# Kernel tuning notes

Hardware: AMD Instinct MI355X
Metric: run time of the kernel (lower is better)

The kernel has to match this reference:

```python
import jax, jax.numpy as jnp
import numpy as np
from jax import lax

B, T, N, H, D = 256, 512, 256, 256, 2  # batch, steps, substrate dim, controller hidden, delay depth
WASHOUT = 64


def setup_inputs() -> dict:
    key = jax.random.key(0)
    ks = jax.random.split(key, 12)
    def w(k, shape, fan_in):
        return (jax.random.normal(k, shape, dtype=jnp.float32) / np.float32(np.sqrt(fan_in)))
    return {
        "settings_seq": jax.random.randint(ks[0], (B, T, 2), 0, 2, dtype=jnp.int32),
        "noise_seq_A": 0.1 * jax.random.normal(ks[1], (B, T, N), dtype=jnp.float32),
        "noise_seq_B": 0.1 * jax.random.normal(ks[2], (B, T, N), dtype=jnp.float32),
        # substrate (two echo-state reservoirs), per-side input = [setting_bit, delayed_logit]
        "W_in_A": w(ks[3], (2, N), 2),
        "W_rec_A": w(ks[4], (N, N), N),
        "W_in_B": w(ks[5], (2, N), 2),
        "W_rec_B": w(ks[6], (N, N), N),
        # controller: single GRU cell over concat(state_A, state_B, spin_A, spin_B) + linear head -> 2 logits
        "Wx": w(ks[7], (2 * N + 2, 3 * H), 2 * N + 2),
        "Wh": w(ks[8], (H, 3 * H), H),
        "b_gru": jnp.zeros((3 * H,), jnp.float32),
        "Wout": w(ks[9], (H, 2), H),
        "b_out": jnp.zeros((2,), jnp.float32),
        "T_total": T,
        "washout_steps": WASHOUT,
    }


def reference(settings_seq, noise_seq_A, noise_seq_B,
              W_in_A, W_rec_A, W_in_B, W_rec_B,
              Wx, Wh, b_gru, Wout, b_out,
              T_total, washout_steps):
    bsz = settings_seq.shape[0]
    h0 = jnp.zeros((bsz, H), jnp.float32)  # controller thought state starts at zeros each step (R <= 1 branch)

    def gru_cell(x, h):
        gx = x @ Wx + b_gru            # [B, 3H]
        gh = h @ Wh                    # [B, 3H] (zero contribution when h == 0)
        z = jax.nn.sigmoid(gx[:, :H] + gh[:, :H])
        r = jax.nn.sigmoid(gx[:, H:2 * H] + gh[:, H:2 * H])
        n = jnp.tanh(gx[:, 2 * H:] + r * gh[:, 2 * H:])
        return (1.0 - z) * n + z * h

    def step(carry, xs):
        sA, sB, buf = carry            # states [B,N], delay buffer [D,B,2]
        nA_t, nB_t, set_t = xs
        bits = set_t.astype(jnp.float32)          # [B,2]
        spins = 2.0 * bits - 1.0                  # bits_to_spins
        x = jnp.concatenate([sA + nA_t, sB + nB_t, spins], axis=-1)
        h = gru_cell(x, h0)
        logits = h @ Wout + b_out                 # [B,2]
        delayed = buf[0]                          # logits from D steps ago
        buf = jnp.concatenate([buf[1:], logits[None]], axis=0)
        inA = jnp.stack([bits[:, 0], delayed[:, 0]], axis=-1)  # [B,2]
        inB = jnp.stack([bits[:, 1], delayed[:, 1]], axis=-1)
        sA = jnp.tanh(inA @ W_in_A + sA @ W_rec_A)
        sB = jnp.tanh(inB @ W_in_B + sB @ W_rec_B)
        return (sA, sB, buf), (jnp.sign(logits), bits)

    init = (jnp.zeros((bsz, N), jnp.float32),
            jnp.zeros((bsz, N), jnp.float32),
            jnp.zeros((D, bsz, 2), jnp.float32))
    xs = (jnp.transpose(noise_seq_A, (1, 0, 2)),
          jnp.transpose(noise_seq_B, (1, 0, 2)),
          jnp.transpose(settings_seq, (1, 0, 2)))
    _, (signs, bits_log) = lax.scan(step, init, xs, length=T_total)
    signs = jnp.transpose(signs, (1, 0, 2))[:, washout_steps:]          # [B, T-washout, 2]
    settings_log = jnp.transpose(bits_log, (1, 0, 2))[:, washout_steps:]
    return signs[..., 0], signs[..., 1], settings_log
```

## Files before the change

kernel.cpp:

```cpp
#include <hip/hip_runtime.h>
#include <cmath>

#define B_ 256
#define T_ 512
#define WASH 64
#define TOUT 448
#define NT 512
#define NBLK 256

#define SRING_OFF 0
#define LRING_OFF 524288
#define SFLAG_OFF 532480
#define LFLAG_OFF 536576

__global__ void init_kernel(float* ws) {
    const int i = blockIdx.x * blockDim.x + threadIdx.x;
    if (i < 8192)
        __hip_atomic_store((unsigned*)(ws + SFLAG_OFF) + i, 0u,
                           __ATOMIC_RELAXED, __HIP_MEMORY_SCOPE_AGENT);
}

__global__ void __launch_bounds__(NT, 2)
loop_kernel(const int* __restrict__ settings, const float* __restrict__ noiseA,
            const float* __restrict__ noiseB, const float* __restrict__ WinA,
            const float* __restrict__ WrecA, const float* __restrict__ WinB,
            const float* __restrict__ WrecB, const float* __restrict__ Wx,
            const float* __restrict__ bg, const float* __restrict__ Wout,
            const float* __restrict__ bout, float* __restrict__ out, float* ws)
{
    __shared__ float part[8][64][17];
    __shared__ float xbuf[516][8];
    __shared__ float sloc[256][4];
    __shared__ float hz[64][9];
    __shared__ float hn[64][9];
    __shared__ float bitsf[4];
    __shared__ float dlybuf[4];

    const int tid = threadIdx.x;
    const int bid = blockIdx.x;
    unsigned* sflag = (unsigned*)(ws + SFLAG_OFF);
    unsigned* lflag = (unsigned*)(ws + LFLAG_OFF);
    float* sring = ws + SRING_OFF;
    float* lring = ws + LRING_OFF;
    float* out0 = out;
    float* out1 = out + (size_t)B_ * TOUT;
    float* out2 = out + (size_t)2 * B_ * TOUT;

    if (bid < 128) {
        const int side = bid & 1, rg4 = bid >> 1;
        const int r0 = rg4 * 4, rg8 = rg4 >> 1, row8b = (rg4 & 1) * 4;
        const int kq = tid >> 6, cg = tid & 63;
        const float* Wr = side ? WrecB : WrecA;
        const float* Wi = side ? WinB : WinA;

        float4 w[32];
        #pragma unroll
        for (int i = 0; i < 32; ++i)
            w[i] = *(const float4*)(Wr + (size_t)(kq * 32 + i) * 256 + cg * 4);

        const int col = tid >> 1, rp = (tid & 1) * 2;
        const float win0 = Wi[col], win1 = Wi[256 + col];
        const float bo = bout[side];

        for (int i = tid; i < 1024; i += NT) ((float*)sloc)[i] = 0.f;
        __syncthreads();

        for (int t = 0; t < T_ + 2; ++t) {
            if (t >= 2 && tid < 4) {
                unsigned* f = lflag + (rg8 * 4 + tid) * 32;
                int g = 0;
                while (__hip_atomic_load(f, __ATOMIC_RELAXED, __HIP_MEMORY_SCOPE_AGENT)
                       < (unsigned)(t - 1)) {
                    __builtin_amdgcn_s_sleep(1);
                    if (++g > 80000) break;
                }
            }
            __syncthreads();

            if (tid < 4) {
                bitsf[tid] = (t < T_)
                    ? (float)settings[((size_t)(r0 + tid) * T_ + t) * 2 + side] : 0.f;
            } else if (tid < 8) {
                const int rr = tid - 4;
                float s = 0.f;
                if (t >= 2) {
                    const float* lb = lring + ((((size_t)((t - 2) & 3)) * 32 + rg8) * 4) * 16
                                      + (row8b + rr) * 2 + side;
                    #pragma unroll
                    for (int cb = 0; cb < 4; ++cb)
                        s += __hip_atomic_load(lb + cb * 16, __ATOMIC_RELAXED,
                                               __HIP_MEMORY_SCOPE_AGENT);
                    s += bo;
                    if (t - 2 >= WASH) {
                        const float sg = (s > 0.f) ? 1.f : ((s < 0.f) ? -1.f : 0.f);
                        __builtin_nontemporal_store(sg,
                            (side ? out1 : out0) + (size_t)(r0 + rr) * TOUT + (t - 2 - WASH));
                    }
                }
                dlybuf[rr] = s;
            }
            if (t < T_) {
                float a00=0,a01=0,a02=0,a03=0, a10=0,a11=0,a12=0,a13=0;
                float a20=0,a21=0,a22=0,a23=0, a30=0,a31=0,a32=0,a33=0;
                #pragma unroll
                for (int i = 0; i < 32; ++i) {
                    const float4 w4 = w[i];
                    const float4 s4 = *(const float4*)&sloc[kq * 32 + i][0];
                    a00 = fmaf(s4.x, w4.x, a00); a10 = fmaf(s4.y, w4.x, a10);
                    a20 = fmaf(s4.z, w4.x, a20); a30 = fmaf(s4.w, w4.x, a30);
                    a01 = fmaf(s4.x, w4.y, a01); a11 = fmaf(s4.y, w4.y, a11);
                    a21 = fmaf(s4.z, w4.y, a21); a31 = fmaf(s4.w, w4.y, a31);
                    a02 = fmaf(s4.x, w4.z, a02); a12 = fmaf(s4.y, w4.z, a12);
                    a22 = fmaf(s4.z, w4.z, a22); a32 = fmaf(s4.w, w4.z, a32);
                    a03 = fmaf(s4.x, w4.w, a03); a13 = fmaf(s4.y, w4.w, a13);
                    a23 = fmaf(s4.z, w4.w, a23); a33 = fmaf(s4.w, w4.w, a33);
                }
                float* pb = &part[kq][cg][0];
                pb[0]=a00; pb[1]=a10; pb[2]=a20; pb[3]=a30;
                pb[4]=a01; pb[5]=a11; pb[6]=a21; pb[7]=a31;
                pb[8]=a02; pb[9]=a12; pb[10]=a22; pb[11]=a32;
                pb[12]=a03; pb[13]=a13; pb[14]=a23; pb[15]=a33;
            }
            __syncthreads();

            if (t < T_) {
                #pragma unroll
                for (int r = 0; r < 2; ++r) {
                    float e = 0.f;
                    #pragma unroll
                    for (int q = 0; q < 8; ++q)
                        e += part[q][col >> 2][(col & 3) * 4 + rp + r];
                    e += bitsf[rp + r] * win0 + dlybuf[rp + r] * win1;
                    sloc[col][rp + r] = tanhf(e);
                }
            }
            __syncthreads();

            if (t < T_) {
                #pragma unroll
                for (int e = 0; e < 2; ++e) {
                    const int idx = tid + e * NT;
                    const int prow = idx >> 8, pcol = idx & 255;
                    __hip_atomic_store(
                        sring + ((size_t)(((t + 1) & 3) * 2 + side) * 256 + r0 + prow) * 256 + pcol,
                        sloc[pcol][prow], __ATOMIC_RELAXED, __HIP_MEMORY_SCOPE_AGENT);
                }
            }
            __syncthreads();
            if (t < T_ && tid == 0) {
                asm volatile("s_waitcnt vmcnt(0)" ::: "memory");
                __hip_atomic_fetch_add(sflag + (side * 64 + rg4) * 32, 1u,
                                       __ATOMIC_RELAXED, __HIP_MEMORY_SCOPE_AGENT);
            }
        }
    } else {
        const int g = bid - 128, rg8 = g >> 2, cb = g & 3, r0 = rg8 * 8;
        const int kq = tid >> 6, c2 = tid & 63;
        const int zcol = cb * 64 + c2, ncol = 512 + zcol;

        float wz[66], wn[66];
        #pragma unroll
        for (int i = 0; i < 66; ++i) {
            const int k = kq * 64 + i;
            const bool v = (i < 64) || (kq == 7);
            wz[i] = v ? Wx[(size_t)k * 768 + zcol] : 0.f;
            wn[i] = v ? Wx[(size_t)k * 768 + ncol] : 0.f;
        }
        const int hd = tid >> 3, rs4 = (tid >> 1) & 3, zn = tid & 1;
        const float bgr = zn ? bg[512 + cb * 64 + hd] : bg[cb * 64 + hd];
        const int wv = tid >> 6, lane = tid & 63, lj = wv & 1;
        const float wo = Wout[(cb * 64 + lane) * 2 + lj];

        const int xk = tid;
        const int sd = (xk < 256) ? 0 : 1;
        const int nc0 = xk & 255;
        const float* npb = (sd ? noiseB : noiseA)
                           + (size_t)r0 * T_ * 256 + nc0;
        float nz[8];
        #pragma unroll
        for (int r = 0; r < 8; ++r) nz[r] = npb[(size_t)r * T_ * 256];

        for (int u = 0; u < T_; ++u) {
            if (u > 0 && tid < 4) {
                unsigned* f = sflag + ((tid & 1) * 64 + rg8 * 2 + (tid >> 1)) * 32;
                int gg = 0;
                while (__hip_atomic_load(f, __ATOMIC_RELAXED, __HIP_MEMORY_SCOPE_AGENT)
                       < (unsigned)u) {
                    __builtin_amdgcn_s_sleep(1);
                    if (++gg > 80000) break;
                }
            }
            __syncthreads();

            {
                float sv[8];
                #pragma unroll
                for (int r = 0; r < 8; ++r) sv[r] = 0.f;
                if (u > 0) {
                    const float* sb = sring
                        + ((size_t)((u & 3) * 2 + sd) * 256 + r0) * 256 + nc0;
                    #pragma unroll
                    for (int r = 0; r < 8; ++r)
                        sv[r] = __hip_atomic_load(sb + (size_t)r * 256,
                                                  __ATOMIC_RELAXED, __HIP_MEMORY_SCOPE_AGENT);
                }
                const int b = (xk >> 2) & 1;
                *(float4*)&xbuf[xk][4 * b] =
                    make_float4(sv[0] + nz[0], sv[1] + nz[1], sv[2] + nz[2], sv[3] + nz[3]);
                *(float4*)&xbuf[xk][4 - 4 * b] =
                    make_float4(sv[4] + nz[4], sv[5] + nz[5], sv[6] + nz[6], sv[7] + nz[7]);
            }
            if (tid < 16) {
                const int rr = tid >> 1, jj = tid & 1;
                const int bv = settings[((size_t)(r0 + rr) * T_ + u) * 2 + jj];
                xbuf[512 + jj][rr] = 2.f * (float)bv - 1.f;
                if (cb == 0 && u >= WASH)
                    __builtin_nontemporal_store((float)bv,
                        out2 + ((size_t)(r0 + rr) * TOUT + (u - WASH)) * 2 + jj);
            }
            __syncthreads();

            {
                const int un = (u + 1 < T_) ? u + 1 : u;
                #pragma unroll
                for (int r = 0; r < 8; ++r)
                    nz[r] = npb[(size_t)r * T_ * 256 + (size_t)un * 256];

                float az0=0,az1=0,az2=0,az3=0,az4=0,az5=0,az6=0,az7=0;
                float an0=0,an1=0,an2=0,an3=0,an4=0,an5=0,an6=0,an7=0;
                #pragma unroll
                for (int i = 0; i < 66; ++i) {
                    const int k = kq * 64 + i;
                    const int bsw = (k >> 2) & 1;
                    const float4 xa = *(const float4*)&xbuf[k][4 * bsw];
                    const float4 xb = *(const float4*)&xbuf[k][4 - 4 * bsw];
                    const float wzi = wz[i], wni = wn[i];
                    az0 = fmaf(xa.x, wzi, az0); az1 = fmaf(xa.y, wzi, az1);
                    az2 = fmaf(xa.z, wzi, az2); az3 = fmaf(xa.w, wzi, az3);
                    az4 = fmaf(xb.x, wzi, az4); az5 = fmaf(xb.y, wzi, az5);
                    az6 = fmaf(xb.z, wzi, az6); az7 = fmaf(xb.w, wzi, az7);
                    an0 = fmaf(xa.x, wni, an0); an1 = fmaf(xa.y, wni, an1);
                    an2 = fmaf(xa.z, wni, an2); an3 = fmaf(xa.w, wni, an3);
                    an4 = fmaf(xb.x, wni, an4); an5 = fmaf(xb.y, wni, an5);
                    an6 = fmaf(xb.z, wni, an6); an7 = fmaf(xb.w, wni, an7);
                }
                float* pb = &part[kq][c2][0];
                pb[0]=az0;  pb[1]=an0;  pb[2]=az1;  pb[3]=an1;
                pb[4]=az2;  pb[5]=an2;  pb[6]=az3;  pb[7]=an3;
                pb[8]=az4;  pb[9]=an4;  pb[10]=az5; pb[11]=an5;
                pb[12]=az6; pb[13]=an6; pb[14]=az7; pb[15]=an7;
            }
            __syncthreads();

            {
                #pragma unroll
                for (int h = 0; h < 2; ++h) {
                    const int rsub = rs4 + h * 4;
                    float e = bgr;
                    #pragma unroll
                    for (int q = 0; q < 8; ++q) e += part[q][hd][rsub * 2 + zn];
                    if (zn == 0) hz[hd][rsub] = 1.f / (1.f + expf(-e));
                    else         hn[hd][rsub] = tanhf(e);
                }
            }
            __syncthreads();

            {
                #pragma unroll
                for (int h = 0; h < 2; ++h) {
                    const int lrow2 = (wv >> 1) + h * 4;
                    float p = (1.f - hz[lane][lrow2]) * hn[lane][lrow2] * wo;
                    #pragma unroll
                    for (int s = 32; s; s >>= 1) p += __shfl_down(p, s, 64);
                    if (lane == 0)
                        __hip_atomic_store(
                            lring + (((size_t)(u & 3) * 32 + rg8) * 4 + cb) * 16 + lrow2 * 2 + lj,
                            p, __ATOMIC_RELAXED, __HIP_MEMORY_SCOPE_AGENT);
                }
            }
            __syncthreads();
            if (tid == 0) {
                asm volatile("s_waitcnt vmcnt(0)" ::: "memory");
                __hip_atomic_fetch_add(lflag + (rg8 * 4 + cb) * 32, 1u,
                                       __ATOMIC_RELAXED, __HIP_MEMORY_SCOPE_AGENT);
            }
        }
    }
}

extern "C" void kernel_launch(void* const* d_in, const int* in_sizes, int n_in,
                              void* d_out, int out_size, void* d_ws, size_t ws_size,
                              hipStream_t stream) {
    (void)in_sizes; (void)n_in; (void)ws_size; (void)out_size;
    float* ws = (float*)d_ws;
    hipLaunchKernelGGL(init_kernel, dim3(32), dim3(256), 0, stream, ws);

    const int*   settings = (const int*)d_in[0];
    const float* noiseA   = (const float*)d_in[1];
    const float* noiseB   = (const float*)d_in[2];
    const float* WinA     = (const float*)d_in[3];
    const float* WrecA    = (const float*)d_in[4];
    const float* WinB     = (const float*)d_in[5];
    const float* WrecB    = (const float*)d_in[6];
    const float* Wx       = (const float*)d_in[7];
    const float* bg       = (const float*)d_in[9];
    const float* Wout     = (const float*)d_in[10];
    const float* bout     = (const float*)d_in[11];
    float*       outp     = (float*)d_out;

    void* args[] = { &settings, &noiseA, &noiseB, &WinA, &WrecA, &WinB, &WrecB,
                     &Wx, &bg, &Wout, &bout, &outp, &ws };
    hipLaunchCooperativeKernel((void*)loop_kernel, dim3(NBLK), dim3(NT),
                               args, 0, stream);
}
```

Before: 3.790 ms.

## Retile GRU gate matvec to 2 columns per thread with 16-way K split

Changes the GRU controller blocks' matvec mapping so each thread owns two z and two n columns over 32 (instead of 64) K rows, with 16 K-partitions. Each xbuf float4 load now feeds 32 FMAs instead of 16, cutting LDS read traffic per FMA. In exchange the partial-sum buffer is larger, and the reduction stage must sum 16 partials instead of 8. Register count per thread changes (136 weights plus 32 accumulators), which may pressure occupancy under the 2-blocks launch bound.

```diff
diff --git a/kernel.cpp b/kernel.cpp
--- a/kernel.cpp
+++ b/kernel.cpp
@@ -28,7 +28,7 @@
             const float* __restrict__ bg, const float* __restrict__ Wout,
             const float* __restrict__ bout, float* __restrict__ out, float* ws)
 {
-    __shared__ float part[8][64][17];
+    __shared__ float part_raw[16 * 32 * 33];
     __shared__ float xbuf[516][8];
     __shared__ float sloc[256][4];
     __shared__ float hz[64][9];
@@ -47,6 +47,7 @@
     float* out2 = out + (size_t)2 * B_ * TOUT;
 
     if (bid < 128) {
+        float (*part)[64][17] = (float (*)[64][17])part_raw;
         const int side = bid & 1, rg4 = bid >> 1;
         const int r0 = rg4 * 4, rg8 = rg4 >> 1, row8b = (rg4 & 1) * 4;
         const int kq = tid >> 6, cg = tid & 63;
@@ -154,20 +155,26 @@
             }
         }
     } else {
+        float (*partG)[32][33] = (float (*)[32][33])part_raw;
         const int g = bid - 128, rg8 = g >> 2, cb = g & 3, r0 = rg8 * 8;
-        const int kq = tid >> 6, c2 = tid & 63;
-        const int zcol = cb * 64 + c2, ncol = 512 + zcol;
-
-        float wz[66], wn[66];
+        const int kq = tid >> 5, cg = tid & 31;
+        const int zc0 = cb * 64 + 2 * cg;
+        const int nc0_ = 512 + zc0;
+
+        float wz0[34], wz1[34], wn0[34], wn1[34];
         #pragma unroll
-        for (int i = 0; i < 66; ++i) {
-            const int k = kq * 64 + i;
-            const bool v = (i < 64) || (kq == 7);
-            wz[i] = v ? Wx[(size_t)k * 768 + zcol] : 0.f;
-            wn[i] = v ? Wx[(size_t)k * 768 + ncol] : 0.f;
+        for (int i = 0; i < 34; ++i) {
+            const int k = kq * 32 + i;
+            const bool v = (i < 32) || (kq == 15);
+            wz0[i] = v ? Wx[(size_t)k * 768 + zc0]      : 0.f;
+            wz1[i] = v ? Wx[(size_t)k * 768 + zc0 + 1]  : 0.f;
+            wn0[i] = v ? Wx[(size_t)k * 768 + nc0_]     : 0.f;
+            wn1[i] = v ? Wx[(size_t)k * 768 + nc0_ + 1] : 0.f;
         }
         const int hd = tid >> 3, rs4 = (tid >> 1) & 3, zn = tid & 1;
         const float bgr = zn ? bg[512 + cb * 64 + hd] : bg[cb * 64 + hd];
+        const int rcg = hd >> 1;
+        const int rci = (zn ? 2 : 0) + (hd & 1);
         const int wv = tid >> 6, lane = tid & 63, lj = wv & 1;
         const float wo = Wout[(cb * 64 + lane) * 2 + lj];
 
@@ -226,29 +233,33 @@
                 for (int r = 0; r < 8; ++r)
                     nz[r] = npb[(size_t)r * T_ * 256 + (size_t)un * 256];
 
-                float az0=0,az1=0,az2=0,az3=0,az4=0,az5=0,az6=0,az7=0;
-                float an0=0,an1=0,an2=0,an3=0,an4=0,an5=0,an6=0,an7=0;
-                #pragma unroll
-                for (int i = 0; i < 66; ++i) {
-                    const int k = kq * 64 + i;
+                float acc[4][8];
+                #pragma unroll
+                for (int c = 0; c < 4; ++c)
+                    #pragma unroll
+                    for (int r = 0; r < 8; ++r) acc[c][r] = 0.f;
+
+                #pragma unroll
+                for (int i = 0; i < 34; ++i) {
+                    const int k = kq * 32 + i;
                     const int bsw = (k >> 2) & 1;
                     const float4 xa = *(const float4*)&xbuf[k][4 * bsw];
                     const float4 xb = *(const float4*)&xbuf[k][4 - 4 * bsw];
-                    const float wzi = wz[i], wni = wn[i];
-                    az0 = fmaf(xa.x, wzi, az0); az1 = fmaf(xa.y, wzi, az1);
-                    az2 = fmaf(xa.z, wzi, az2); az3 = fmaf(xa.w, wzi, az3);
-                    az4 = fmaf(xb.x, wzi, az4); az5 = fmaf(xb.y, wzi, az5);
-                    az6 = fmaf(xb.z, wzi, az6); az7 = fmaf(xb.w, wzi, az7);
-                    an0 = fmaf(xa.x, wni, an0); an1 = fmaf(xa.y, wni, an1);
-                    an2 = fmaf(xa.z, wni, an2); an3 = fmaf(xa.w, wni, an3);
-                    an4 = fmaf(xb.x, wni, an4); an5 = fmaf(xb.y, wni, an5);
-                    an6 = fmaf(xb.z, wni, an6); an7 = fmaf(xb.w, wni, an7);
-                }
-                float* pb = &part[kq][c2][0];
-                pb[0]=az0;  pb[1]=an0;  pb[2]=az1;  pb[3]=an1;
-                pb[4]=az2;  pb[5]=an2;  pb[6]=az3;  pb[7]=an3;
-                pb[8]=az4;  pb[9]=an4;  pb[10]=az5; pb[11]=an5;
-                pb[12]=az6; pb[13]=an6; pb[14]=az7; pb[15]=an7;
+                    const float xr[8] = { xa.x, xa.y, xa.z, xa.w,
+                                          xb.x, xb.y, xb.z, xb.w };
+                    const float wv4[4] = { wz0[i], wz1[i], wn0[i], wn1[i] };
+                    #pragma unroll
+                    for (int c = 0; c < 4; ++c)
+                        #pragma unroll
+                        for (int r = 0; r < 8; ++r)
+                            acc[c][r] = fmaf(xr[r], wv4[c], acc[c][r]);
+                }
+                float* pb = &partG[kq][cg][0];
+                #pragma unroll
+                for (int c = 0; c < 4; ++c)
+                    #pragma unroll
+                    for (int r = 0; r < 8; ++r)
+                        pb[c * 8 + r] = acc[c][r];
             }
             __syncthreads();
 
@@ -258,7 +269,8 @@
                     const int rsub = rs4 + h * 4;
                     float e = bgr;
                     #pragma unroll
-                    for (int q = 0; q < 8; ++q) e += part[q][hd][rsub * 2 + zn];
+                    for (int q = 0; q < 16; ++q)
+                        e += partG[q][rcg][rci * 8 + rsub];
                     if (zn == 0) hz[hd][rsub] = 1.f / (1.f + expf(-e));
                     else         hn[hd][rsub] = tanhf(e);
                 }
```

Result: slower. 8.987 ms (+137.2%).

## Speculatively prefetch next-step substrate state in GRU blocks and cache flag polls

Applied to the files above, without the earlier changes.

The GRU blocks now poll the substrate ready-flags during the current step's matvec. When all four flags already show the next step is ready, they load the next substrate state and settings and fill xbuf in the tail of the current iteration. This removes the separate spin-wait, the global load phase and one barrier from the next iteration. Both block types also cache the last observed flag value so they skip polling when the producer is known to be ahead. The cost is extra control logic and registers for the prefetched values, with a fallback to the original blocking path when the data is not ready.

```diff
diff --git a/kernel.cpp b/kernel.cpp
--- a/kernel.cpp
+++ b/kernel.cpp
@@ -28,13 +28,14 @@
             const float* __restrict__ bg, const float* __restrict__ Wout,
             const float* __restrict__ bout, float* __restrict__ out, float* ws)
 {
-    __shared__ float part[8][64][17];
+    __shared__ float part_raw[8 * 64 * 17];
     __shared__ float xbuf[516][8];
     __shared__ float sloc[256][4];
     __shared__ float hz[64][9];
     __shared__ float hn[64][9];
     __shared__ float bitsf[4];
     __shared__ float dlybuf[4];
+    __shared__ int   grdy[4];
 
     const int tid = threadIdx.x;
     const int bid = blockIdx.x;
@@ -47,6 +48,7 @@
     float* out2 = out + (size_t)2 * B_ * TOUT;
 
     if (bid < 128) {
+        float (*part)[64][17] = (float (*)[64][17])part_raw;
         const int side = bid & 1, rg4 = bid >> 1;
         const int r0 = rg4 * 4, rg8 = rg4 >> 1, row8b = (rg4 & 1) * 4;
         const int kq = tid >> 6, cg = tid & 63;
@@ -65,11 +67,13 @@
         for (int i = tid; i < 1024; i += NT) ((float*)sloc)[i] = 0.f;
         __syncthreads();
 
+        unsigned lcache = 0;
         for (int t = 0; t < T_ + 2; ++t) {
-            if (t >= 2 && tid < 4) {
+            if (t >= 2 && tid < 4 && lcache < (unsigned)(t - 1)) {
                 unsigned* f = lflag + (rg8 * 4 + tid) * 32;
                 int g = 0;
-                while (__hip_atomic_load(f, __ATOMIC_RELAXED, __HIP_MEMORY_SCOPE_AGENT)
+                while ((lcache = __hip_atomic_load(f, __ATOMIC_RELAXED,
+                                                   __HIP_MEMORY_SCOPE_AGENT))
                        < (unsigned)(t - 1)) {
                     __builtin_amdgcn_s_sleep(1);
                     if (++g > 80000) break;
@@ -154,6 +158,7 @@
             }
         }
     } else {
+        float (*partG)[64][17] = (float (*)[64][17])part_raw;
         const int g = bid - 128, rg8 = g >> 2, cb = g & 3, r0 = rg8 * 8;
         const int kq = tid >> 6, c2 = tid & 63;
         const int zcol = cb * 64 + c2, ncol = 512 + zcol;
@@ -174,57 +179,76 @@
         const int xk = tid;
         const int sd = (xk < 256) ? 0 : 1;
         const int nc0 = xk & 255;
-        const float* npb = (sd ? noiseB : noiseA)
-                           + (size_t)r0 * T_ * 256 + nc0;
+        const float* npb = (sd ? noiseB : noiseA) + (size_t)r0 * T_ * 256 + nc0;
         float nz[8];
         #pragma unroll
         for (int r = 0; r < 8; ++r) nz[r] = npb[(size_t)r * T_ * 256];
 
+        unsigned* myf = sflag + (((tid & 1) * 64) + rg8 * 2 + ((tid >> 1) & 1)) * 32;
+        unsigned scache = 0;
+
+        {
+            const int b = (xk >> 2) & 1;
+            *(float4*)&xbuf[xk][4 * b]     = make_float4(nz[0], nz[1], nz[2], nz[3]);
+            *(float4*)&xbuf[xk][4 - 4 * b] = make_float4(nz[4], nz[5], nz[6], nz[7]);
+        }
+        int sreg = 0;
+        if (tid < 16) {
+            const int rr = tid >> 1, jj = tid & 1;
+            sreg = settings[((size_t)(r0 + rr) * T_) * 2 + jj];
+            xbuf[512 + jj][rr] = 2.f * (float)sreg - 1.f;
+        }
+        __syncthreads();
+        bool rdy = true;
+
         for (int u = 0; u < T_; ++u) {
-            if (u > 0 && tid < 4) {
-                unsigned* f = sflag + ((tid & 1) * 64 + rg8 * 2 + (tid >> 1)) * 32;
-                int gg = 0;
-                while (__hip_atomic_load(f, __ATOMIC_RELAXED, __HIP_MEMORY_SCOPE_AGENT)
-                       < (unsigned)u) {
-                    __builtin_amdgcn_s_sleep(1);
-                    if (++gg > 80000) break;
-                }
-            }
-            __syncthreads();
-
-            {
-                float sv[8];
-                #pragma unroll
-                for (int r = 0; r < 8; ++r) sv[r] = 0.f;
-                if (u > 0) {
+            if (!rdy) {
+                if (tid < 4 && scache < (unsigned)u) {
+                    int gg = 0;
+                    while ((scache = __hip_atomic_load(myf, __ATOMIC_RELAXED,
+                                                       __HIP_MEMORY_SCOPE_AGENT))
+                           < (unsigned)u) {
+                        __builtin_amdgcn_s_sleep(1);
+                        if (++gg > 80000) break;
+                    }
+                }
+                __syncthreads();
+                {
                     const float* sb = sring
                         + ((size_t)((u & 3) * 2 + sd) * 256 + r0) * 256 + nc0;
+                    float sv[8];
                     #pragma unroll
                     for (int r = 0; r < 8; ++r)
                         sv[r] = __hip_atomic_load(sb + (size_t)r * 256,
                                                   __ATOMIC_RELAXED, __HIP_MEMORY_SCOPE_AGENT);
-                }
-                const int b = (xk >> 2) & 1;
-                *(float4*)&xbuf[xk][4 * b] =
-                    make_float4(sv[0] + nz[0], sv[1] + nz[1], sv[2] + nz[2], sv[3] + nz[3]);
-                *(float4*)&xbuf[xk][4 - 4 * b] =
-                    make_float4(sv[4] + nz[4], sv[5] + nz[5], sv[6] + nz[6], sv[7] + nz[7]);
-            }
-            if (tid < 16) {
-                const int rr = tid >> 1, jj = tid & 1;
-                const int bv = settings[((size_t)(r0 + rr) * T_ + u) * 2 + jj];
-                xbuf[512 + jj][rr] = 2.f * (float)bv - 1.f;
-                if (cb == 0 && u >= WASH)
-                    __builtin_nontemporal_store((float)bv,
-                        out2 + ((size_t)(r0 + rr) * TOUT + (u - WASH)) * 2 + jj);
-            }
-            __syncthreads();
+                    const int b = (xk >> 2) & 1;
+                    *(float4*)&xbuf[xk][4 * b] =
+                        make_float4(sv[0] + nz[0], sv[1] + nz[1], sv[2] + nz[2], sv[3] + nz[3]);
+                    *(float4*)&xbuf[xk][4 - 4 * b] =
+                        make_float4(sv[4] + nz[4], sv[5] + nz[5], sv[6] + nz[6], sv[7] + nz[7]);
+                }
+                if (tid < 16) {
+                    const int rr = tid >> 1, jj = tid & 1;
+                    xbuf[512 + jj][rr] = 2.f * (float)sreg - 1.f;
+                    if (cb == 0 && u >= WASH)
+                        __builtin_nontemporal_store((float)sreg,
+                            out2 + ((size_t)(r0 + rr) * TOUT + (u - WASH)) * 2 + jj);
+                }
+                __syncthreads();
+            }
 
             {
                 const int un = (u + 1 < T_) ? u + 1 : u;
                 #pragma unroll
                 for (int r = 0; r < 8; ++r)
                     nz[r] = npb[(size_t)r * T_ * 256 + (size_t)un * 256];
+                if (tid < 16 && u + 1 < T_) {
+                    const int rr = tid >> 1, jj = tid & 1;
+                    sreg = settings[((size_t)(r0 + rr) * T_ + (u + 1)) * 2 + jj];
+                }
+                if (tid < 4 && scache < (unsigned)(u + 1))
+                    scache = __hip_atomic_load(myf, __ATOMIC_RELAXED,
+                                               __HIP_MEMORY_SCOPE_AGENT);
 
                 float az0=0,az1=0,az2=0,az3=0,az4=0,az5=0,az6=0,az7=0;
                 float an0=0,an1=0,an2=0,an3=0,an4=0,an5=0,an6=0,an7=0;
@@ -244,21 +268,33 @@
                     an4 = fmaf(xb.x, wni, an4); an5 = fmaf(xb.y, wni, an5);
                     an6 = fmaf(xb.z, wni, an6); an7 = fmaf(xb.w, wni, an7);
                 }
-                float* pb = &part[kq][c2][0];
+                float* pb = &partG[kq][c2][0];
                 pb[0]=az0;  pb[1]=an0;  pb[2]=az1;  pb[3]=an1;
                 pb[4]=az2;  pb[5]=an2;  pb[6]=az3;  pb[7]=an3;
                 pb[8]=az4;  pb[9]=an4;  pb[10]=az5; pb[11]=an5;
                 pb[12]=az6; pb[13]=an6; pb[14]=az7; pb[15]=an7;
-            }
-            __syncthreads();
-
+                if (tid < 4) grdy[tid] = (scache >= (unsigned)(u + 1)) ? 1 : 0;
+            }
+            __syncthreads();
+
+            const bool rdyn = (u + 1 < T_) &&
+                              grdy[0] && grdy[1] && grdy[2] && grdy[3];
+            float sv[8];
+            if (rdyn) {
+                const float* sb = sring
+                    + ((size_t)(((u + 1) & 3) * 2 + sd) * 256 + r0) * 256 + nc0;
+                #pragma unroll
+                for (int r = 0; r < 8; ++r)
+                    sv[r] = __hip_atomic_load(sb + (size_t)r * 256,
+                                              __ATOMIC_RELAXED, __HIP_MEMORY_SCOPE_AGENT);
+            }
             {
                 #pragma unroll
                 for (int h = 0; h < 2; ++h) {
                     const int rsub = rs4 + h * 4;
                     float e = bgr;
                     #pragma unroll
-                    for (int q = 0; q < 8; ++q) e += part[q][hd][rsub * 2 + zn];
+                    for (int q = 0; q < 8; ++q) e += partG[q][hd][rsub * 2 + zn];
                     if (zn == 0) hz[hd][rsub] = 1.f / (1.f + expf(-e));
                     else         hn[hd][rsub] = tanhf(e);
                 }
@@ -278,12 +314,27 @@
                             p, __ATOMIC_RELAXED, __HIP_MEMORY_SCOPE_AGENT);
                 }
             }
+            if (rdyn) {
+                const int b = (xk >> 2) & 1;
+                *(float4*)&xbuf[xk][4 * b] =
+                    make_float4(sv[0] + nz[0], sv[1] + nz[1], sv[2] + nz[2], sv[3] + nz[3]);
+                *(float4*)&xbuf[xk][4 - 4 * b] =
+                    make_float4(sv[4] + nz[4], sv[5] + nz[5], sv[6] + nz[6], sv[7] + nz[7]);
+                if (tid < 16) {
+                    const int rr = tid >> 1, jj = tid & 1;
+                    xbuf[512 + jj][rr] = 2.f * (float)sreg - 1.f;
+                    if (cb == 0 && u + 1 >= WASH)
+                        __builtin_nontemporal_store((float)sreg,
+                            out2 + ((size_t)(r0 + rr) * TOUT + (u + 1 - WASH)) * 2 + jj);
+                }
+            }
             __syncthreads();
             if (tid == 0) {
                 asm volatile("s_waitcnt vmcnt(0)" ::: "memory");
                 __hip_atomic_fetch_add(lflag + (rg8 * 4 + cb) * 32, 1u,
                                        __ATOMIC_RELAXED, __HIP_MEMORY_SCOPE_AGENT);
             }
+            rdy = rdyn;
         }
     }
 }
```

After: 5.348 ms. 41.1% more time.
